# Kernel optimization log

Hardware: AMD Instinct MI355X
Metric: run time of the kernel (lower is better)

Reference implementation:

```python
import jax, jax.numpy as jnp
import numpy as np

PARAMETER = 0.1
INPUT_SIZE = 512
OUTPUT_SIZE = 512


def setup_inputs() -> dict:
    key = jax.random.key(0)
    k1, k2, k3 = jax.random.split(key, 3)
    T, B = 4096, 32
    input_tensor = jax.random.normal(k1, (T, B, INPUT_SIZE), dtype=jnp.float32)
    k = np.sqrt(1.0 / INPUT_SIZE)
    weight = jax.random.uniform(k2, (OUTPUT_SIZE, INPUT_SIZE), dtype=jnp.float32, minval=-k, maxval=k)
    bias = jax.random.uniform(k3, (OUTPUT_SIZE,), dtype=jnp.float32, minval=-k, maxval=k)
    return {"input_tensor": input_tensor, "weight": weight, "bias": bias}


def reference(input_tensor, weight, bias):
    # linear projection: [T, B, I] @ [I, O] -> [T, B, O]
    y = jnp.einsum('tbi,oi->tbo', input_tensor, weight) + bias

    # EMA recurrence: v[0] = y[0]; v[t] = p * v[t-1] + y[t]
    def step(carry, yt):
        v = PARAMETER * carry + yt
        return v, v

    _, rest = jax.lax.scan(step, y[0], y[1:])
    return jnp.concatenate([y[:1], rest], axis=0)
```

## Files before the change

### kernel.cpp

```cpp
#include <hip/hip_runtime.h>
#include <hip/hip_bf16.h>

#define T_DIM 4096
#define B_DIM 32
#define I_DIM 512
#define O_DIM 512
#define M_DIM (T_DIM * B_DIM)
#define PARAM 0.1f
#define ISCALE 1.1111112f

#define STRIP 32
#define TAPS 8

#define BM 256
#define BN 256
#define BK 64
#define NK (I_DIM / BK)

typedef __attribute__((ext_vector_type(8))) short bf16x8;
typedef __attribute__((ext_vector_type(4))) float f32x4;

__device__ __forceinline__ unsigned short f2bf(float f) {
    union { __hip_bfloat16 b; unsigned short u; } cv;
    cv.b = __float2bfloat16(f);
    return cv.u;
}

__global__ __launch_bounds__(256) void wcvt_kernel(const float* __restrict__ W,
                                                   unsigned short* __restrict__ Wb) {
    const int i = (blockIdx.x * 256 + threadIdx.x) * 4;
    f32x4 v = *(const f32x4*)(W + i);
    ushort4 o;
    o.x = f2bf(v[0]); o.y = f2bf(v[1]); o.z = f2bf(v[2]); o.w = f2bf(v[3]);
    *(ushort4*)(Wb + i) = o;
}

__global__ __launch_bounds__(256) void xema_kernel(const float* __restrict__ X,
                                                   unsigned short* __restrict__ Xv) {
    const int s   = blockIdx.x >> 4;
    const int blk = blockIdx.x & 15;
    const int col = (blk * 256 + threadIdx.x) * 4;
    const int t0  = s * STRIP;
    const int b   = col >> 9;
    const int o   = col & 511;

    const float* xin = X + (size_t)t0 * 16384 + col;
    unsigned short* xout = Xv + (size_t)(t0 * 32 + b) * 512 + o;

    f32x4 v = {0.f, 0.f, 0.f, 0.f};
    if (s > 0) {
        const float* w = xin - (size_t)TAPS * 16384;
        #pragma unroll
        for (int j = 0; j < TAPS; ++j)
            v = PARAM * v + *(const f32x4*)(w + (size_t)j * 16384);
    }

    f32x4 bufA[4], bufB[4];
    #pragma unroll
    for (int j = 0; j < 4; ++j) bufA[j] = *(const f32x4*)(xin + (size_t)j * 16384);

    #pragma unroll
    for (int i = 0; i < STRIP; i += 8) {
        #pragma unroll
        for (int j = 0; j < 4; ++j)
            bufB[j] = *(const f32x4*)(xin + (size_t)(i + 4 + j) * 16384);
        #pragma unroll
        for (int j = 0; j < 4; ++j) {
            v = PARAM * v + bufA[j];
            ushort4 pk; pk.x = f2bf(v[0]); pk.y = f2bf(v[1]); pk.z = f2bf(v[2]); pk.w = f2bf(v[3]);
            *(ushort4*)(xout + (size_t)(i + j) * 16384) = pk;
        }
        if (i + 8 < STRIP) {
            #pragma unroll
            for (int j = 0; j < 4; ++j)
                bufA[j] = *(const f32x4*)(xin + (size_t)(i + 8 + j) * 16384);
        }
        #pragma unroll
        for (int j = 0; j < 4; ++j) {
            v = PARAM * v + bufB[j];
            ushort4 pk; pk.x = f2bf(v[0]); pk.y = f2bf(v[1]); pk.z = f2bf(v[2]); pk.w = f2bf(v[3]);
            *(ushort4*)(xout + (size_t)(i + 4 + j) * 16384) = pk;
        }
    }
}

__global__ __launch_bounds__(512, 2) void gemm_kernel(const unsigned short* __restrict__ Xv,
                                                      const unsigned short* __restrict__ Wb,
                                                      const float* __restrict__ bias,
                                                      float* __restrict__ Y) {
    __shared__ __align__(16) short As[2][BM * BK];
    __shared__ __align__(16) short Bs[2][BN * BK];

    const int tid  = threadIdx.x;
    const int lane = tid & 63;
    const int wave = tid >> 6;
    const int wm   = wave >> 2;
    const int wn   = wave & 3;

    const int bid  = blockIdx.x;
    const int swz  = (bid & 7) * 128 + (bid >> 3);
    const int bn   = swz & 1;
    const int mt   = swz >> 1;
    const int row0 = mt * BM;
    const int col0 = bn * BN;

    const int cs = (tid & 7) ^ ((tid >> 3) & 7);
    const unsigned short* aSrc = Xv + (size_t)(row0 + (tid >> 3)) * 512 + cs * 8;
    const unsigned short* bSrc = Wb + (size_t)(col0 + (tid >> 3)) * 512 + cs * 8;

    #define STAGE(d, kt)                                                              \
        do {                                                                          \
            _Pragma("unroll")                                                         \
            for (int s_ = 0; s_ < 4; ++s_)                                            \
                __builtin_amdgcn_global_load_lds(                                     \
                    (const __attribute__((address_space(1))) unsigned int*)(aSrc + (size_t)s_ * 64 * 512 + (kt) * 64), \
                    (__attribute__((address_space(3))) unsigned int*)(&As[d][0] + (s_ * 512 + tid) * 8),              \
                    16, 0, 0);                                                        \
            _Pragma("unroll")                                                         \
            for (int s_ = 0; s_ < 4; ++s_)                                            \
                __builtin_amdgcn_global_load_lds(                                     \
                    (const __attribute__((address_space(1))) unsigned int*)(bSrc + (size_t)s_ * 64 * 512 + (kt) * 64), \
                    (__attribute__((address_space(3))) unsigned int*)(&Bs[d][0] + (s_ * 512 + tid) * 8),              \
                    16, 0, 0);                                                        \
        } while (0)

    f32x4 acc[8][4] = {};

    STAGE(0, 0);
    __syncthreads();

    for (int ks = 0; ks < NK; ++ks) {
        const int cur = ks & 1;
        if (ks < NK - 1)
            STAGE(cur ^ 1, ks + 1);

        #pragma unroll
        for (int kk = 0; kk < 2; ++kk) {
            const int cc = kk * 4 + (lane >> 4);
            bf16x8 a_[8], b_[4];
            #pragma unroll
            for (int mf = 0; mf < 8; ++mf) {
                const int r = wm * 128 + mf * 16 + (lane & 15);
                a_[mf] = *(const bf16x8*)((const char*)&As[cur][0] + r * 128 + ((cc ^ (r & 7)) << 4));
            }
            #pragma unroll
            for (int nf = 0; nf < 4; ++nf) {
                const int r = wn * 64 + nf * 16 + (lane & 15);
                b_[nf] = *(const bf16x8*)((const char*)&Bs[cur][0] + r * 128 + ((cc ^ (r & 7)) << 4));
            }
            #pragma unroll
            for (int mf = 0; mf < 8; ++mf)
                #pragma unroll
                for (int nf = 0; nf < 4; ++nf)
                    acc[mf][nf] = __builtin_amdgcn_mfma_f32_16x16x32_bf16(
                        b_[nf], a_[mf], acc[mf][nf], 0, 0, 0);
        }
        __syncthreads();
    }

    float sc4[4];
    #pragma unroll
    for (int tt = 0; tt < 4; ++tt) {
        const int t_ = ((row0 + wm * 128) >> 5) + tt;
        sc4[tt] = (1.0f - __expf(-2.3025851f * (float)(t_ + 1))) * ISCALE;
    }
    f32x4 bvv[4];
    #pragma unroll
    for (int nf = 0; nf < 4; ++nf)
        bvv[nf] = *(const f32x4*)(bias + col0 + wn * 64 + nf * 16 + ((lane >> 4) << 2));

    #pragma unroll
    for (int mf = 0; mf < 8; ++mf) {
        const int grow = row0 + wm * 128 + mf * 16 + (lane & 15);
        const float sc = sc4[mf >> 1];
        #pragma unroll
        for (int nf = 0; nf < 4; ++nf) {
            const int gcol = col0 + wn * 64 + nf * 16 + ((lane >> 4) << 2);
            f32x4 out;
            #pragma unroll
            for (int e = 0; e < 4; ++e) out[e] = acc[mf][nf][e] + sc * bvv[nf][e];
            *(f32x4*)(Y + (size_t)grow * O_DIM + gcol) = out;
        }
    }
}

extern "C" void kernel_launch(void* const* d_in, const int* in_sizes, int n_in,
                              void* d_out, int out_size, void* d_ws, size_t ws_size,
                              hipStream_t stream) {
    const float* X    = (const float*)d_in[0];
    const float* W    = (const float*)d_in[1];
    const float* bias = (const float*)d_in[2];
    float* Y = (float*)d_out;
    unsigned short* Wb = (unsigned short*)d_ws;
    unsigned short* Xv = (unsigned short*)((char*)d_ws + (1 << 20));

    wcvt_kernel<<<dim3(O_DIM * I_DIM / (256 * 4)), dim3(256), 0, stream>>>(W, Wb);
    xema_kernel<<<dim3((T_DIM / STRIP) * 16), dim3(256), 0, stream>>>(X, Xv);
    gemm_kernel<<<dim3((M_DIM / BM) * (O_DIM / BN)), dim3(512), 0, stream>>>(Xv, Wb, bias, Y);
}
```

Measured before the change: 235.9 us.

## Fuse input EMA and bf16 conversion into GEMM A-tile staging

Removes the separate xema kernel and its bf16 intermediate buffer. Each GEMM block now loads the fp32 input rows itself, runs the truncated 8-tap EMA warm-up plus 8 output steps in registers, and writes bf16 directly into the swizzled LDS A tile. The N tile shrinks from 256 to 128, so there are four column blocks per M tile. This avoids a round trip of the bf16 Xv tensor through global memory, but each X element is now read and EMA-computed by four column blocks, with 16 fp32 loads per thread per k-step and double the halo rows.

After: 271.5 us. 15.1% more time.

```diff
diff --git a/kernel.cpp b/kernel.cpp
--- a/kernel.cpp
+++ b/kernel.cpp
@@ -9,11 +9,8 @@
 #define PARAM 0.1f
 #define ISCALE 1.1111112f
 
-#define STRIP 32
-#define TAPS 8
-
 #define BM 256
-#define BN 256
+#define BN 128
 #define BK 64
 #define NK (I_DIM / BK)
 
@@ -35,59 +32,10 @@
     *(ushort4*)(Wb + i) = o;
 }
 
-__global__ __launch_bounds__(256) void xema_kernel(const float* __restrict__ X,
-                                                   unsigned short* __restrict__ Xv) {
-    const int s   = blockIdx.x >> 4;
-    const int blk = blockIdx.x & 15;
-    const int col = (blk * 256 + threadIdx.x) * 4;
-    const int t0  = s * STRIP;
-    const int b   = col >> 9;
-    const int o   = col & 511;
-
-    const float* xin = X + (size_t)t0 * 16384 + col;
-    unsigned short* xout = Xv + (size_t)(t0 * 32 + b) * 512 + o;
-
-    f32x4 v = {0.f, 0.f, 0.f, 0.f};
-    if (s > 0) {
-        const float* w = xin - (size_t)TAPS * 16384;
-        #pragma unroll
-        for (int j = 0; j < TAPS; ++j)
-            v = PARAM * v + *(const f32x4*)(w + (size_t)j * 16384);
-    }
-
-    f32x4 bufA[4], bufB[4];
-    #pragma unroll
-    for (int j = 0; j < 4; ++j) bufA[j] = *(const f32x4*)(xin + (size_t)j * 16384);
-
-    #pragma unroll
-    for (int i = 0; i < STRIP; i += 8) {
-        #pragma unroll
-        for (int j = 0; j < 4; ++j)
-            bufB[j] = *(const f32x4*)(xin + (size_t)(i + 4 + j) * 16384);
-        #pragma unroll
-        for (int j = 0; j < 4; ++j) {
-            v = PARAM * v + bufA[j];
-            ushort4 pk; pk.x = f2bf(v[0]); pk.y = f2bf(v[1]); pk.z = f2bf(v[2]); pk.w = f2bf(v[3]);
-            *(ushort4*)(xout + (size_t)(i + j) * 16384) = pk;
-        }
-        if (i + 8 < STRIP) {
-            #pragma unroll
-            for (int j = 0; j < 4; ++j)
-                bufA[j] = *(const f32x4*)(xin + (size_t)(i + 8 + j) * 16384);
-        }
-        #pragma unroll
-        for (int j = 0; j < 4; ++j) {
-            v = PARAM * v + bufB[j];
-            ushort4 pk; pk.x = f2bf(v[0]); pk.y = f2bf(v[1]); pk.z = f2bf(v[2]); pk.w = f2bf(v[3]);
-            *(ushort4*)(xout + (size_t)(i + 4 + j) * 16384) = pk;
-        }
-    }
-}
-
-__global__ __launch_bounds__(512, 2) void gemm_kernel(const unsigned short* __restrict__ Xv,
-                                                      const unsigned short* __restrict__ Wb,
-                                                      const float* __restrict__ bias,
-                                                      float* __restrict__ Y) {
+__global__ __launch_bounds__(512, 2) void fused_kernel(const float* __restrict__ X,
+                                                       const unsigned short* __restrict__ Wb,
+                                                       const float* __restrict__ bias,
+                                                       float* __restrict__ Y) {
     __shared__ __align__(16) short As[2][BM * BK];
     __shared__ __align__(16) short Bs[2][BN * BK];
 
@@ -97,91 +45,139 @@
     const int wm   = wave >> 2;
     const int wn   = wave & 3;
 
-    const int bid  = blockIdx.x;
-    const int swz  = (bid & 7) * 128 + (bid >> 3);
-    const int bn   = swz & 1;
-    const int mt   = swz >> 1;
+    const int bid = blockIdx.x;
+    const int swz = (bid & 7) * 256 + (bid >> 3);
+    const int bn  = swz & 3;
+    const int mt  = swz >> 2;
     const int row0 = mt * BM;
     const int col0 = bn * BN;
+    const int t0   = mt * 8;
 
     const int cs = (tid & 7) ^ ((tid >> 3) & 7);
-    const unsigned short* aSrc = Xv + (size_t)(row0 + (tid >> 3)) * 512 + cs * 8;
     const unsigned short* bSrc = Wb + (size_t)(col0 + (tid >> 3)) * 512 + cs * 8;
 
-    #define STAGE(d, kt)                                                              \
+    #define STAGE_B(d, kt)                                                            \
         do {                                                                          \
             _Pragma("unroll")                                                         \
-            for (int s_ = 0; s_ < 4; ++s_)                                            \
-                __builtin_amdgcn_global_load_lds(                                     \
-                    (const __attribute__((address_space(1))) unsigned int*)(aSrc + (size_t)s_ * 64 * 512 + (kt) * 64), \
-                    (__attribute__((address_space(3))) unsigned int*)(&As[d][0] + (s_ * 512 + tid) * 8),              \
-                    16, 0, 0);                                                        \
-            _Pragma("unroll")                                                         \
-            for (int s_ = 0; s_ < 4; ++s_)                                            \
+            for (int s_ = 0; s_ < 2; ++s_)                                            \
                 __builtin_amdgcn_global_load_lds(                                     \
                     (const __attribute__((address_space(1))) unsigned int*)(bSrc + (size_t)s_ * 64 * 512 + (kt) * 64), \
                     (__attribute__((address_space(3))) unsigned int*)(&Bs[d][0] + (s_ * 512 + tid) * 8),              \
                     16, 0, 0);                                                        \
         } while (0)
 
-    f32x4 acc[8][4] = {};
+    const int bb = tid >> 4;
+    const int kq = tid & 15;
+    const float* xBase = X + (size_t)bb * 512 + kq * 4;
+    const int aw = (((kq >> 1) ^ (bb & 7)) << 4) + ((kq & 1) << 3);
 
-    STAGE(0, 0);
+    f32x4 xr[16];
+
+    #define XLOAD(ks_)                                                                \
+        do {                                                                          \
+            const float* xp = xBase + (size_t)(ks_) * 64;                             \
+            if (t0 >= 8) {                                                            \
+                _Pragma("unroll")                                                     \
+                for (int j_ = 0; j_ < 16; ++j_)                                       \
+                    xr[j_] = *(const f32x4*)(xp + (size_t)(t0 - 8 + j_) * 16384);     \
+            } else {                                                                  \
+                _Pragma("unroll")                                                     \
+                for (int j_ = 0; j_ < 16; ++j_) {                                     \
+                    const int t_ = t0 - 8 + j_;                                       \
+                    if (t_ >= 0) xr[j_] = *(const f32x4*)(xp + (size_t)t_ * 16384);   \
+                    else         xr[j_] = (f32x4){0.f, 0.f, 0.f, 0.f};                \
+                }                                                                     \
+            }                                                                         \
+        } while (0)
+
+    #define EMA_WRITE(d)                                                              \
+        do {                                                                          \
+            f32x4 v_ = xr[0];                                                         \
+            _Pragma("unroll")                                                         \
+            for (int j_ = 1; j_ < 8; ++j_) v_ = PARAM * v_ + xr[j_];                  \
+            _Pragma("unroll")                                                         \
+            for (int tl = 0; tl < 8; ++tl) {                                          \
+                v_ = PARAM * v_ + xr[8 + tl];                                         \
+                ushort4 pk_;                                                          \
+                pk_.x = f2bf(v_[0]); pk_.y = f2bf(v_[1]);                             \
+                pk_.z = f2bf(v_[2]); pk_.w = f2bf(v_[3]);                             \
+                *(ushort4*)((char*)&As[d][0] + (tl * 32 + bb) * 128 + aw) = pk_;      \
+            }                                                                         \
+        } while (0)
+
+    f32x4 acc[8][2] = {};
+
+    #define COMPUTE(d)                                                                \
+        do {                                                                          \
+            _Pragma("unroll")                                                         \
+            for (int kk = 0; kk < 2; ++kk) {                                          \
+                const int cc = kk * 4 + (lane >> 4);                                  \
+                bf16x8 a_[8], b_[2];                                                  \
+                _Pragma("unroll")                                                     \
+                for (int mf = 0; mf < 8; ++mf) {                                      \
+                    const int r = wm * 128 + mf * 16 + (lane & 15);                   \
+                    a_[mf] = *(const bf16x8*)((const char*)&As[d][0] + r * 128 + ((cc ^ (r & 7)) << 4)); \
+                }                                                                     \
+                _Pragma("unroll")                                                     \
+                for (int nf = 0; nf < 2; ++nf) {                                      \
+                    const int r = wn * 32 + nf * 16 + (lane & 15);                    \
+                    b_[nf] = *(const bf16x8*)((const char*)&Bs[d][0] + r * 128 + ((cc ^ (r & 7)) << 4)); \
+                }                                                                     \
+                _Pragma("unroll")                                                     \
+                for (int mf = 0; mf < 8; ++mf)                                        \
+                    _Pragma("unroll")                                                 \
+                    for (int nf = 0; nf < 2; ++nf)                                    \
+                        acc[mf][nf] = __builtin_amdgcn_mfma_f32_16x16x32_bf16(        \
+                            b_[nf], a_[mf], acc[mf][nf], 0, 0, 0);                    \
+            }                                                                         \
+        } while (0)
+
+    STAGE_B(0, 0);
+    XLOAD(0);
+    EMA_WRITE(0);
     __syncthreads();
 
+    #pragma unroll
     for (int ks = 0; ks < NK; ++ks) {
         const int cur = ks & 1;
+        if (ks < NK - 1) {
+            STAGE_B(cur ^ 1, ks + 1);
+            XLOAD(ks + 1);
+        }
+        COMPUTE(cur);
         if (ks < NK - 1)
-            STAGE(cur ^ 1, ks + 1);
-
-        #pragma unroll
-        for (int kk = 0; kk < 2; ++kk) {
-            const int cc = kk * 4 + (lane >> 4);
-            bf16x8 a_[8], b_[4];
-            #pragma unroll
-            for (int mf = 0; mf < 8; ++mf) {
-                const int r = wm * 128 + mf * 16 + (lane & 15);
-                a_[mf] = *(const bf16x8*)((const char*)&As[cur][0] + r * 128 + ((cc ^ (r & 7)) << 4));
-            }
-            #pragma unroll
-            for (int nf = 0; nf < 4; ++nf) {
-                const int r = wn * 64 + nf * 16 + (lane & 15);
-                b_[nf] = *(const bf16x8*)((const char*)&Bs[cur][0] + r * 128 + ((cc ^ (r & 7)) << 4));
-            }
-            #pragma unroll
-            for (int mf = 0; mf < 8; ++mf)
-                #pragma unroll
-                for (int nf = 0; nf < 4; ++nf)
-                    acc[mf][nf] = __builtin_amdgcn_mfma_f32_16x16x32_bf16(
-                        b_[nf], a_[mf], acc[mf][nf], 0, 0, 0);
-        }
+            EMA_WRITE(cur ^ 1);
         __syncthreads();
     }
 
     float sc4[4];
     #pragma unroll
     for (int tt = 0; tt < 4; ++tt) {
-        const int t_ = ((row0 + wm * 128) >> 5) + tt;
+        const int t_ = t0 + wm * 4 + tt;
         sc4[tt] = (1.0f - __expf(-2.3025851f * (float)(t_ + 1))) * ISCALE;
     }
-    f32x4 bvv[4];
+    f32x4 bvv[2];
     #pragma unroll
-    for (int nf = 0; nf < 4; ++nf)
-        bvv[nf] = *(const f32x4*)(bias + col0 + wn * 64 + nf * 16 + ((lane >> 4) << 2));
+    for (int nf = 0; nf < 2; ++nf)
+        bvv[nf] = *(const f32x4*)(bias + col0 + wn * 32 + nf * 16 + ((lane >> 4) << 2));
 
     #pragma unroll
     for (int mf = 0; mf < 8; ++mf) {
         const int grow = row0 + wm * 128 + mf * 16 + (lane & 15);
         const float sc = sc4[mf >> 1];
         #pragma unroll
-        for (int nf = 0; nf < 4; ++nf) {
-            const int gcol = col0 + wn * 64 + nf * 16 + ((lane >> 4) << 2);
+        for (int nf = 0; nf < 2; ++nf) {
+            const int gcol = col0 + wn * 32 + nf * 16 + ((lane >> 4) << 2);
             f32x4 out;
             #pragma unroll
             for (int e = 0; e < 4; ++e) out[e] = acc[mf][nf][e] + sc * bvv[nf][e];
             *(f32x4*)(Y + (size_t)grow * O_DIM + gcol) = out;
         }
     }
+    #undef STAGE_B
+    #undef XLOAD
+    #undef EMA_WRITE
+    #undef COMPUTE
 }
 
 extern "C" void kernel_launch(void* const* d_in, const int* in_sizes, int n_in,
@@ -192,9 +188,7 @@
     const float* bias = (const float*)d_in[2];
     float* Y = (float*)d_out;
     unsigned short* Wb = (unsigned short*)d_ws;
-    unsigned short* Xv = (unsigned short*)((char*)d_ws + (1 << 20));
 
     wcvt_kernel<<<dim3(O_DIM * I_DIM / (256 * 4)), dim3(256), 0, stream>>>(W, Wb);
-    xema_kernel<<<dim3((T_DIM / STRIP) * 16), dim3(256), 0, stream>>>(X, Xv);
-    gemm_kernel<<<dim3((M_DIM / BM) * (O_DIM / BN)), dim3(512), 0, stream>>>(Xv, Wb, bias, Y);
+    fused_kernel<<<dim3((M_DIM / BM) * (O_DIM / BN)), dim3(512), 0, stream>>>(X, Wb, bias, Y);
 }
```
